# Kernel optimization log

Hardware: AMD Instinct MI355X
Metric: run time of the kernel (lower is better)

The kernel has to match this reference:

```python
import jax, jax.numpy as jnp
import numpy as np

N = 2048      # nodes (= in_features = out_features, forced by h0 @ adj)
C = 512       # channels
B = 8         # batch
NNZ = 65536   # number of edges (avg degree 32)
NEG = -9e15   # masked-fill value from the source


def setup_inputs() -> dict:
    key = jax.random.key(0)
    k1, k2, k3, k4 = jax.random.split(key, 4)
    x = jax.random.normal(k1, (B, C, N), dtype=jnp.float32)
    # xavier_normal_ with gain=0.01: std = gain * sqrt(2/(fan_in+fan_out))
    std = 0.01 * float(np.sqrt(2.0 / (N + N)))
    W1 = jax.random.normal(k2, (N, N), dtype=jnp.float32) * std
    W2 = jax.random.normal(k3, (N, N), dtype=jnp.float32) * std
    # e is initialized to 1 in the source; perturb so softmax is non-trivial
    e = 1.0 + 0.1 * jax.random.normal(k4, (NNZ,), dtype=jnp.float32)
    # flat row-major indices of mask nonzeros, unique + sorted (matches adj[mask] = e)
    rng = np.random.default_rng(0)
    edge_idx = np.sort(rng.choice(N * N, size=NNZ, replace=False)).astype(np.int64)
    return {"x": x, "W1": W1, "W2": W2, "e": e, "edge_idx": jnp.asarray(edge_idx)}


def reference(x, W1, W2, e, edge_idx):
    # h0, h1: [B, C, N]
    h0 = jnp.matmul(x, W1)
    h1 = jnp.matmul(x, W2)
    # scatter per-edge logits into dense [N, N], masked positions = -9e15
    logits = jnp.full((N * N,), NEG, dtype=jnp.float32).at[edge_idx].set(e)
    A = jax.nn.softmax(logits.reshape(N, N), axis=1)  # row-wise softmax
    diag = jnp.diagonal(A)                 # A * I  (self term, diagonal scaling)
    A_off = A - jnp.diag(diag)             # A * (1 - I)  (neighbor term)
    # h0 @ (A*I) == h0 scaled per-node by diag; h1 @ (A*(1-I)) dense GEMM
    out = h0 * diag[None, None, :] + jnp.matmul(h1, A_off)
    return out  # [B, C, N]; torch squeeze is a no-op here; bias=False
```

## Files before the change

kernel.cpp:

```cpp
#include <hip/hip_runtime.h>
#include <hip/hip_bf16.h>
#include <stdint.h>

#define NN 2048
#define LOG2NN 11
#define GK 2048
#define GNC 2048

typedef __bf16 bf16x8 __attribute__((ext_vector_type(8)));
typedef float f32x4 __attribute__((ext_vector_type(4)));

__device__ __forceinline__ ushort f2bf(float f) {
  uint32_t x = __float_as_uint(f);
  uint32_t r = (x + 0x7fffu + ((x >> 16) & 1u)) >> 16;
  return (ushort)r;
}

__global__ __launch_bounds__(256) void prep_kernel(
    const float* __restrict__ W1, const float* __restrict__ W2,
    ushort* __restrict__ WT, ushort* __restrict__ W2T,
    const float* __restrict__ x, ushort* __restrict__ xb,
    int* __restrict__ hist, float* __restrict__ uW, int* __restrict__ ecnt) {
  __shared__ float tile[64][65];
  const int bid = blockIdx.x;
  const int t = threadIdx.x;
  if (bid < 2048) {
    const int m = bid >> 10;
    const int rem = bid & 1023;
    const int r0 = (rem >> 5) * 64, c0 = (rem & 31) * 64;
    const float* in = m ? W2 : W1;
    ushort* out = m ? W2T : WT;
    const int tx = t & 15, ty = t >> 4;
#pragma unroll
    for (int i = 0; i < 4; ++i) {
      int r = i * 16 + ty;
      float4 v = *reinterpret_cast<const float4*>(&in[(size_t)(r0 + r) * NN + c0 + tx * 4]);
      tile[r][tx * 4 + 0] = v.x;
      tile[r][tx * 4 + 1] = v.y;
      tile[r][tx * 4 + 2] = v.z;
      tile[r][tx * 4 + 3] = v.w;
    }
    __syncthreads();
#pragma unroll
    for (int i = 0; i < 4; ++i) {
      int oc = i * 16 + ty;
      ushort4 o;
      o.x = f2bf(tile[tx * 4 + 0][oc]);
      o.y = f2bf(tile[tx * 4 + 1][oc]);
      o.z = f2bf(tile[tx * 4 + 2][oc]);
      o.w = f2bf(tile[tx * 4 + 3][oc]);
      *reinterpret_cast<ushort4*>(&out[(size_t)(c0 + oc) * NN + r0 + tx * 4]) = o;
    }
  } else if (bid < 6144) {
    int i = (bid - 2048) * 256 + t;
    const float4* in4 = reinterpret_cast<const float4*>(x);
    float4 a = in4[2 * i];
    float4 b = in4[2 * i + 1];
    uint4 o;
    o.x = (uint32_t)f2bf(a.x) | ((uint32_t)f2bf(a.y) << 16);
    o.y = (uint32_t)f2bf(a.z) | ((uint32_t)f2bf(a.w) << 16);
    o.z = (uint32_t)f2bf(b.x) | ((uint32_t)f2bf(b.y) << 16);
    o.w = (uint32_t)f2bf(b.z) | ((uint32_t)f2bf(b.w) << 16);
    reinterpret_cast<uint4*>(xb)[i] = o;
  } else {
#pragma unroll
    for (int j = 0; j < 8; ++j) {
      hist[t * 8 + j] = 0;
      uW[t * 8 + j] = 0.f;
    }
    if (t == 0) *ecnt = 0;
  }
}

__device__ __forceinline__ int lower_bound32(const int* __restrict__ a, int n, int v) {
  int lo = 0, hi = n;
  while (lo < hi) {
    int mid = (lo + hi) >> 1;
    if (a[mid] < v) lo = mid + 1; else hi = mid;
  }
  return lo;
}

__global__ __launch_bounds__(256) void softmax_hist_kernel(
    const int* __restrict__ idx, const float* __restrict__ e, int nnz,
    float* __restrict__ vals, float* __restrict__ diag, int* __restrict__ empty,
    int* __restrict__ ecnt, int* __restrict__ hist) {
  const int w = threadIdx.x >> 6, lane = threadIdx.x & 63;
  const int r = blockIdx.x * 4 + w;
  int lo = lower_bound32(idx, nnz, r << LOG2NN);
  int hi = lower_bound32(idx, nnz, (r + 1) << LOG2NN);
  if (hi <= lo) {
    if (lane == 0) { diag[r] = 1.0f / NN; empty[r] = 1; atomicAdd(ecnt, 1); }
    return;
  }
  float m = -3.0e38f;
  for (int j = lo + lane; j < hi; j += 64) m = fmaxf(m, e[j]);
#pragma unroll
  for (int s = 32; s >= 1; s >>= 1) m = fmaxf(m, __shfl_xor(m, s));
  float sum = 0.f;
  for (int j = lo + lane; j < hi; j += 64) sum += expf(e[j] - m);
#pragma unroll
  for (int s = 32; s >= 1; s >>= 1) sum += __shfl_xor(sum, s);
  float inv = 1.0f / sum;
  float dv = 0.f;
  for (int j = lo + lane; j < hi; j += 64) {
    float v = expf(e[j] - m) * inv;
    vals[j] = v;
    int c = idx[j] & (NN - 1);
    if (c == r) dv = v;
    else atomicAdd(&hist[c], 1);
  }
#pragma unroll
  for (int s = 32; s >= 1; s >>= 1) dv += __shfl_xor(dv, s);
  if (lane == 0) { diag[r] = dv; empty[r] = 0; }
}

__global__ __launch_bounds__(256) void scan_uw_kernel(
    const int* __restrict__ hist, int* __restrict__ base, int* __restrict__ cursor,
    const float* __restrict__ W2, const int* __restrict__ empty,
    const int* __restrict__ ecnt, float* __restrict__ uW) {
  if (blockIdx.x == 0) {
    const int l = threadIdx.x;
    if (l >= 64) return;
    int vals[32], pre[32];
    int run = 0;
#pragma unroll
    for (int j = 0; j < 32; ++j) {
      vals[j] = hist[l * 32 + j];
      pre[j] = run;
      run += vals[j];
    }
    int tot = run, inc = run;
#pragma unroll
    for (int s = 1; s < 64; s <<= 1) {
      int o = __shfl_up(inc, s);
      if (l >= s) inc += o;
    }
    int excl = inc - tot;
#pragma unroll
    for (int j = 0; j < 32; ++j) {
      int b = excl + pre[j];
      base[l * 32 + j] = b;
      cursor[l * 32 + j] = b;
    }
  } else {
    if (*ecnt == 0) return;
    int p = (blockIdx.x - 1) * 256 + threadIdx.x;
    float s = 0.f;
    for (int k = 0; k < NN; ++k)
      if (empty[k]) s += W2[(size_t)p * NN + k];
    uW[p] = s * (1.0f / NN);
  }
}

__global__ void scatter_kernel(const int* __restrict__ idx, const float* __restrict__ vals,
                               int nnz, int* __restrict__ cursor,
                               int* __restrict__ ek, float* __restrict__ ev) {
  int j = blockIdx.x * blockDim.x + threadIdx.x;
  if (j >= nnz) return;
  int f = idx[j];
  int c = f & (NN - 1), r = f >> LOG2NN;
  if (c != r) {
    int p = atomicAdd(&cursor[c], 1);
    ek[p] = r;
    ev[p] = vals[j];
  }
}

__global__ __launch_bounds__(256) void spmm_kernel(
    const int* __restrict__ ek, const float* __restrict__ ev,
    const int* __restrict__ base, const int* __restrict__ hist,
    const ushort* __restrict__ W2T,
    const float* __restrict__ diag, const int* __restrict__ empty,
    const float* __restrict__ uW, ushort* WT) {
  const int w = threadIdx.x >> 6, lane = threadIdx.x & 63;
  const int n = blockIdx.x * 2 + (w >> 1);
  const int c0 = (w & 1) * 1024 + lane * 16;
  const int start = base[n], cnt = hist[n];
  float acc[2][8];
#pragma unroll
  for (int g = 0; g < 2; ++g) {
    float4 u0 = *reinterpret_cast<const float4*>(&uW[c0 + g * 8]);
    float4 u1 = *reinterpret_cast<const float4*>(&uW[c0 + g * 8 + 4]);
    acc[g][0] = u0.x; acc[g][1] = u0.y; acc[g][2] = u0.z; acc[g][3] = u0.w;
    acc[g][4] = u1.x; acc[g][5] = u1.y; acc[g][6] = u1.z; acc[g][7] = u1.w;
  }
  float d = diag[n];
  if (d != 0.f) {
#pragma unroll
    for (int g = 0; g < 2; ++g) {
      bf16x8 wd = *reinterpret_cast<const bf16x8*>(&WT[(size_t)n * NN + c0 + g * 8]);
#pragma unroll
      for (int j = 0; j < 8; ++j) acc[g][j] += d * (float)wd[j];
    }
  }
  int i = 0;
  for (; i + 4 <= cnt; i += 4) {
    int k[4];
    float v[4];
    bf16x8 wv[4][2];
#pragma unroll
    for (int e2 = 0; e2 < 4; ++e2) {
      k[e2] = ek[start + i + e2];
      v[e2] = ev[start + i + e2];
    }
#pragma unroll
    for (int e2 = 0; e2 < 4; ++e2)
#pragma unroll
      for (int g = 0; g < 2; ++g)
        wv[e2][g] = *reinterpret_cast<const bf16x8*>(&W2T[(size_t)k[e2] * NN + c0 + g * 8]);
#pragma unroll
    for (int e2 = 0; e2 < 4; ++e2)
#pragma unroll
      for (int g = 0; g < 2; ++g)
#pragma unroll
        for (int j = 0; j < 8; ++j)
          acc[g][j] += v[e2] * (float)wv[e2][g][j];
  }
  for (; i < cnt; ++i) {
    int k0 = ek[start + i];
    float v0 = ev[start + i];
#pragma unroll
    for (int g = 0; g < 2; ++g) {
      bf16x8 w0 = *reinterpret_cast<const bf16x8*>(&W2T[(size_t)k0 * NN + c0 + g * 8]);
#pragma unroll
      for (int j = 0; j < 8; ++j) acc[g][j] += v0 * (float)w0[j];
    }
  }
  if (empty[n]) {
#pragma unroll
    for (int g = 0; g < 2; ++g) {
      bf16x8 we = *reinterpret_cast<const bf16x8*>(&W2T[(size_t)n * NN + c0 + g * 8]);
#pragma unroll
      for (int j = 0; j < 8; ++j) acc[g][j] -= (1.0f / NN) * (float)we[j];
    }
  }
#pragma unroll
  for (int g = 0; g < 2; ++g) {
    uint4 o;
    o.x = (uint32_t)f2bf(acc[g][0]) | ((uint32_t)f2bf(acc[g][1]) << 16);
    o.y = (uint32_t)f2bf(acc[g][2]) | ((uint32_t)f2bf(acc[g][3]) << 16);
    o.z = (uint32_t)f2bf(acc[g][4]) | ((uint32_t)f2bf(acc[g][5]) << 16);
    o.w = (uint32_t)f2bf(acc[g][6]) | ((uint32_t)f2bf(acc[g][7]) << 16);
    *reinterpret_cast<uint4*>(&WT[(size_t)n * NN + c0 + g * 8]) = o;
  }
}

__device__ __forceinline__ void gload_lds16(const ushort* g, char* l) {
  __builtin_amdgcn_global_load_lds(
      (__attribute__((address_space(1))) uint32_t*)(uintptr_t)g,
      (__attribute__((address_space(3))) uint32_t*)l, 16, 0, 0);
}

#define NT 32

__global__ __launch_bounds__(512, 2)
void gemm8_kernel(const ushort* __restrict__ A, const ushort* __restrict__ Bt,
                  float* __restrict__ Cf) {
  __shared__ __align__(16) char smem[98304];
  const int t = threadIdx.x;
  const int wid = t >> 6, lane = t & 63;
  const int wm = wid >> 2, wn = wid & 3;
  const int fr = lane & 15, fg = lane >> 4;

  const int swz = ((int)blockIdx.x & 7) * 32 + ((int)blockIdx.x >> 3);
  const int m0 = (swz >> 4) * 256;
  const int n0 = (swz & 15) * 128;

  const int l8 = lane >> 3;
  const int scol = ((lane & 7) ^ l8) << 3;
  const int srow = wid * 8 + l8;

#define STGA(H, TAU) do {                                                      \
    const int _b = (TAU) & 1;                                                  \
    gload_lds16(A + (size_t)(m0 + (H) * 128 + srow) * GK + (TAU) * 64 + scol,  \
                smem + _b * 32768 + (H) * 16384 + wid * 1024);                 \
    gload_lds16(A + (size_t)(m0 + (H) * 128 + 64 + srow) * GK + (TAU) * 64 + scol, \
                smem + _b * 32768 + (H) * 16384 + 8192 + wid * 1024);          \
  } while (0)

#define STGB(TAU) do {                                                         \
    const int _b = (TAU) & 1;                                                  \
    gload_lds16(Bt + (size_t)(n0 + srow) * GK + (TAU) * 64 + scol,             \
                smem + 65536 + _b * 16384 + wid * 1024);                       \
    gload_lds16(Bt + (size_t)(n0 + 64 + srow) * GK + (TAU) * 64 + scol,        \
                smem + 65536 + _b * 16384 + 8192 + wid * 1024);                \
  } while (0)

  const int sw = (fr & 7) << 4;
  const int ko0 = (fg * 16) ^ sw;
  const int ko1 = (64 + fg * 16) ^ sw;
  const int arow = (wm * 16 + fr) * 128;
  const int brow = (wn * 32 + fr) * 128;

  f32x4 acc[2][4][2] = {};
  bf16x8 aF[4][2], bF[2][2];

#define LDA(MQ, B_) do {                                                       \
    _Pragma("unroll") for (int mf = 0; mf < 4; ++mf) {                         \
      const char* _p = smem + (B_) * 32768 + arow + ((MQ) * 128 + mf * 32) * 128; \
      aF[mf][0] = *reinterpret_cast<const bf16x8*>(_p + ko0);                  \
      aF[mf][1] = *reinterpret_cast<const bf16x8*>(_p + ko1);                  \
    }                                                                          \
  } while (0)

#define LDB(B_) do {                                                           \
    _Pragma("unroll") for (int nf = 0; nf < 2; ++nf) {                         \
      const char* _p = smem + 65536 + (B_) * 16384 + brow + (nf * 16) * 128;   \
      bF[nf][0] = *reinterpret_cast<const bf16x8*>(_p + ko0);                  \
      bF[nf][1] = *reinterpret_cast<const bf16x8*>(_p + ko1);                  \
    }                                                                          \
  } while (0)

#define MM(MQ) do {                                                            \
    _Pragma("unroll") for (int mf = 0; mf < 4; ++mf)                           \
      _Pragma("unroll") for (int nf = 0; nf < 2; ++nf) {                       \
        acc[MQ][mf][nf] = __builtin_amdgcn_mfma_f32_16x16x32_bf16(             \
            aF[mf][0], bF[nf][0], acc[MQ][mf][nf], 0, 0, 0);                   \
        acc[MQ][mf][nf] = __builtin_amdgcn_mfma_f32_16x16x32_bf16(             \
            aF[mf][1], bF[nf][1], acc[MQ][mf][nf], 0, 0, 0);                   \
      }                                                                        \
  } while (0)

#define PHASE_MID() do {                                                       \
    __builtin_amdgcn_s_barrier();                                              \
    asm volatile("s_waitcnt lgkmcnt(0)" ::: "memory");                         \
    __builtin_amdgcn_sched_barrier(0);                                         \
    __builtin_amdgcn_s_setprio(1);                                             \
  } while (0)

#define PHASE_END() do {                                                       \
    __builtin_amdgcn_s_setprio(0);                                             \
    __builtin_amdgcn_s_barrier();                                              \
  } while (0)

  STGA(0, 0); STGA(1, 0); STGB(0);
  STGB(1); STGA(0, 1);
  asm volatile("s_waitcnt vmcnt(4)" ::: "memory");
  __builtin_amdgcn_sched_barrier(0);
  __builtin_amdgcn_s_barrier();

  for (int kt = 0; kt < NT; ++kt) {
    const int b = kt & 1;
    const int t1 = (kt + 1) & (NT - 1), t2 = (kt + 2) & (NT - 1);
    LDA(0, b); LDB(b);
    STGA(1, t1);
    PHASE_MID(); MM(0); PHASE_END();
    LDA(1, b);
    STGB(t2); STGA(0, t2);
    PHASE_MID(); MM(1);
    __builtin_amdgcn_s_setprio(0);
    asm volatile("s_waitcnt vmcnt(4)" ::: "memory");
    __builtin_amdgcn_sched_barrier(0);
    __builtin_amdgcn_s_barrier();
  }

  asm volatile("s_waitcnt vmcnt(0)" ::: "memory");
  const int cr = lane >> 4, cc = lane & 15;
#pragma unroll
  for (int mq = 0; mq < 2; ++mq)
#pragma unroll
    for (int mf = 0; mf < 4; ++mf)
#pragma unroll
      for (int nf = 0; nf < 2; ++nf)
#pragma unroll
        for (int q = 0; q < 4; ++q) {
          int gm = m0 + mq * 128 + mf * 32 + wm * 16 + cr * 4 + q;
          int gn = n0 + wn * 32 + nf * 16 + cc;
          Cf[(size_t)gm * GNC + gn] = acc[mq][mf][nf][q];
        }
}

extern "C" void kernel_launch(void* const* d_in, const int* in_sizes, int n_in,
                              void* d_out, int out_size, void* d_ws, size_t ws_size,
                              hipStream_t stream) {
  const float* x   = (const float*)d_in[0];
  const float* W1  = (const float*)d_in[1];
  const float* W2  = (const float*)d_in[2];
  const float* e   = (const float*)d_in[3];
  const int*   eix = (const int*)d_in[4];
  const int nnz = in_sizes[3];
  float* out = (float*)d_out;

  char* w = (char*)d_ws;
  ushort* W2T  = (ushort*)w; w += (size_t)NN * NN * 2;
  ushort* WT   = (ushort*)w; w += (size_t)NN * NN * 2;
  ushort* xb   = (ushort*)w; w += (size_t)4096 * NN * 2;
  float*  vals = (float*)w;  w += (size_t)nnz * 4;
  int*    ek   = (int*)w;    w += (size_t)nnz * 4;
  float*  ev   = (float*)w;  w += (size_t)nnz * 4;
  int*    hist = (int*)w;    w += NN * 4;
  int*    base = (int*)w;    w += NN * 4;
  int*    curs = (int*)w;    w += NN * 4;
  float*  diag = (float*)w;  w += NN * 4;
  int*    empt = (int*)w;    w += NN * 4;
  float*  uW   = (float*)w;  w += NN * 4;
  int*    ecnt = (int*)w;    w += 256;

  prep_kernel<<<dim3(6145), dim3(256), 0, stream>>>(W1, W2, WT, W2T, x, xb,
                                                    hist, uW, ecnt);
  softmax_hist_kernel<<<dim3(512), dim3(256), 0, stream>>>(eix, e, nnz, vals,
                                                           diag, empt, ecnt, hist);
  scan_uw_kernel<<<dim3(9), dim3(256), 0, stream>>>(hist, base, curs, W2, empt,
                                                    ecnt, uW);
  scatter_kernel<<<dim3((nnz + 255) / 256), dim3(256), 0, stream>>>(eix, vals, nnz,
                                                                    curs, ek, ev);
  spmm_kernel<<<dim3(1024), dim3(256), 0, stream>>>(ek, ev, base, hist, W2T,
                                                    diag, empt, uW, WT);
  gemm8_kernel<<<dim3(256), dim3(512), 0, stream>>>(xb, WT, out);
}
```

Measured before the change: 109.7 us.

## Fuse softmax into prep kernel, move x conversion into spmm, restructure GEMM warp tiling

The row-softmax/histogram work moves into the prep kernel as extra blocks, and the zeroing of hist, uW and ecnt becomes a single memset. The x-to-bf16 conversion moves out of prep and into extra blocks of the spmm kernel, dropping one launch and letting that conversion run alongside the sparse work. The GEMM main loop changes from a two-phase split with finer barriers to one loop per k-tile, with each wave computing a 64x64 sub-tile (4x4 MFMA fragments) instead of 2x(4x2). It loads then waits for the next stage only after the compute, which gives up some of the earlier overlap between loads and MFMAs.

```diff
diff --git a/kernel.cpp b/kernel.cpp
--- a/kernel.cpp
+++ b/kernel.cpp
@@ -16,11 +16,21 @@
   return (ushort)r;
 }
 
+__device__ __forceinline__ int lower_bound32(const int* __restrict__ a, int n, int v) {
+  int lo = 0, hi = n;
+  while (lo < hi) {
+    int mid = (lo + hi) >> 1;
+    if (a[mid] < v) lo = mid + 1; else hi = mid;
+  }
+  return lo;
+}
+
 __global__ __launch_bounds__(256) void prep_kernel(
     const float* __restrict__ W1, const float* __restrict__ W2,
     ushort* __restrict__ WT, ushort* __restrict__ W2T,
-    const float* __restrict__ x, ushort* __restrict__ xb,
-    int* __restrict__ hist, float* __restrict__ uW, int* __restrict__ ecnt) {
+    int* __restrict__ hist, int* __restrict__ ecnt,
+    const int* __restrict__ idx, const float* __restrict__ e, int nnz,
+    float* __restrict__ vals, float* __restrict__ diag, int* __restrict__ empty) {
   __shared__ float tile[64][65];
   const int bid = blockIdx.x;
   const int t = threadIdx.x;
@@ -51,68 +61,36 @@
       o.w = f2bf(tile[tx * 4 + 3][oc]);
       *reinterpret_cast<ushort4*>(&out[(size_t)(c0 + oc) * NN + r0 + tx * 4]) = o;
     }
-  } else if (bid < 6144) {
-    int i = (bid - 2048) * 256 + t;
-    const float4* in4 = reinterpret_cast<const float4*>(x);
-    float4 a = in4[2 * i];
-    float4 b = in4[2 * i + 1];
-    uint4 o;
-    o.x = (uint32_t)f2bf(a.x) | ((uint32_t)f2bf(a.y) << 16);
-    o.y = (uint32_t)f2bf(a.z) | ((uint32_t)f2bf(a.w) << 16);
-    o.z = (uint32_t)f2bf(b.x) | ((uint32_t)f2bf(b.y) << 16);
-    o.w = (uint32_t)f2bf(b.z) | ((uint32_t)f2bf(b.w) << 16);
-    reinterpret_cast<uint4*>(xb)[i] = o;
   } else {
-#pragma unroll
-    for (int j = 0; j < 8; ++j) {
-      hist[t * 8 + j] = 0;
-      uW[t * 8 + j] = 0.f;
-    }
-    if (t == 0) *ecnt = 0;
-  }
-}
-
-__device__ __forceinline__ int lower_bound32(const int* __restrict__ a, int n, int v) {
-  int lo = 0, hi = n;
-  while (lo < hi) {
-    int mid = (lo + hi) >> 1;
-    if (a[mid] < v) lo = mid + 1; else hi = mid;
-  }
-  return lo;
-}
-
-__global__ __launch_bounds__(256) void softmax_hist_kernel(
-    const int* __restrict__ idx, const float* __restrict__ e, int nnz,
-    float* __restrict__ vals, float* __restrict__ diag, int* __restrict__ empty,
-    int* __restrict__ ecnt, int* __restrict__ hist) {
-  const int w = threadIdx.x >> 6, lane = threadIdx.x & 63;
-  const int r = blockIdx.x * 4 + w;
-  int lo = lower_bound32(idx, nnz, r << LOG2NN);
-  int hi = lower_bound32(idx, nnz, (r + 1) << LOG2NN);
-  if (hi <= lo) {
-    if (lane == 0) { diag[r] = 1.0f / NN; empty[r] = 1; atomicAdd(ecnt, 1); }
-    return;
-  }
-  float m = -3.0e38f;
-  for (int j = lo + lane; j < hi; j += 64) m = fmaxf(m, e[j]);
-#pragma unroll
-  for (int s = 32; s >= 1; s >>= 1) m = fmaxf(m, __shfl_xor(m, s));
-  float sum = 0.f;
-  for (int j = lo + lane; j < hi; j += 64) sum += expf(e[j] - m);
-#pragma unroll
-  for (int s = 32; s >= 1; s >>= 1) sum += __shfl_xor(sum, s);
-  float inv = 1.0f / sum;
-  float dv = 0.f;
-  for (int j = lo + lane; j < hi; j += 64) {
-    float v = expf(e[j] - m) * inv;
-    vals[j] = v;
-    int c = idx[j] & (NN - 1);
-    if (c == r) dv = v;
-    else atomicAdd(&hist[c], 1);
-  }
-#pragma unroll
-  for (int s = 32; s >= 1; s >>= 1) dv += __shfl_xor(dv, s);
-  if (lane == 0) { diag[r] = dv; empty[r] = 0; }
+    const int w = t >> 6, lane = t & 63;
+    const int r = (bid - 2048) * 4 + w;
+    int lo = lower_bound32(idx, nnz, r << LOG2NN);
+    int hi = lower_bound32(idx, nnz, (r + 1) << LOG2NN);
+    if (hi <= lo) {
+      if (lane == 0) { diag[r] = 1.0f / NN; empty[r] = 1; atomicAdd(ecnt, 1); }
+      return;
+    }
+    float m = -3.0e38f;
+    for (int j = lo + lane; j < hi; j += 64) m = fmaxf(m, e[j]);
+#pragma unroll
+    for (int s = 32; s >= 1; s >>= 1) m = fmaxf(m, __shfl_xor(m, s));
+    float sum = 0.f;
+    for (int j = lo + lane; j < hi; j += 64) sum += expf(e[j] - m);
+#pragma unroll
+    for (int s = 32; s >= 1; s >>= 1) sum += __shfl_xor(sum, s);
+    float inv = 1.0f / sum;
+    float dv = 0.f;
+    for (int j = lo + lane; j < hi; j += 64) {
+      float v = expf(e[j] - m) * inv;
+      vals[j] = v;
+      int c = idx[j] & (NN - 1);
+      if (c == r) dv = v;
+      else atomicAdd(&hist[c], 1);
+    }
+#pragma unroll
+    for (int s = 32; s >= 1; s >>= 1) dv += __shfl_xor(dv, s);
+    if (lane == 0) { diag[r] = dv; empty[r] = 0; }
+  }
 }
 
 __global__ __launch_bounds__(256) void scan_uw_kernel(
@@ -172,7 +150,21 @@
     const int* __restrict__ base, const int* __restrict__ hist,
     const ushort* __restrict__ W2T,
     const float* __restrict__ diag, const int* __restrict__ empty,
-    const float* __restrict__ uW, ushort* WT) {
+    const float* __restrict__ uW, ushort* WT,
+    const float* __restrict__ x, ushort* __restrict__ xb) {
+  if (blockIdx.x >= 1024) {
+    int i = ((int)blockIdx.x - 1024) * 256 + threadIdx.x;
+    const float4* in4 = reinterpret_cast<const float4*>(x);
+    float4 a = in4[2 * i];
+    float4 b = in4[2 * i + 1];
+    uint4 o;
+    o.x = (uint32_t)f2bf(a.x) | ((uint32_t)f2bf(a.y) << 16);
+    o.y = (uint32_t)f2bf(a.z) | ((uint32_t)f2bf(a.w) << 16);
+    o.z = (uint32_t)f2bf(b.x) | ((uint32_t)f2bf(b.y) << 16);
+    o.w = (uint32_t)f2bf(b.z) | ((uint32_t)f2bf(b.w) << 16);
+    reinterpret_cast<uint4*>(xb)[i] = o;
+    return;
+  }
   const int w = threadIdx.x >> 6, lane = threadIdx.x & 63;
   const int n = blockIdx.x * 2 + (w >> 1);
   const int c0 = (w & 1) * 1024 + lane * 16;
@@ -260,7 +252,7 @@
   __shared__ __align__(16) char smem[98304];
   const int t = threadIdx.x;
   const int wid = t >> 6, lane = t & 63;
-  const int wm = wid >> 2, wn = wid & 3;
+  const int wm = wid >> 1, wn = wid & 1;
   const int fr = lane & 15, fg = lane >> 4;
 
   const int swz = ((int)blockIdx.x & 7) * 32 + ((int)blockIdx.x >> 3);
@@ -290,85 +282,77 @@
   const int sw = (fr & 7) << 4;
   const int ko0 = (fg * 16) ^ sw;
   const int ko1 = (64 + fg * 16) ^ sw;
-  const int arow = (wm * 16 + fr) * 128;
-  const int brow = (wn * 32 + fr) * 128;
-
-  f32x4 acc[2][4][2] = {};
-  bf16x8 aF[4][2], bF[2][2];
-
-#define LDA(MQ, B_) do {                                                       \
-    _Pragma("unroll") for (int mf = 0; mf < 4; ++mf) {                         \
-      const char* _p = smem + (B_) * 32768 + arow + ((MQ) * 128 + mf * 32) * 128; \
-      aF[mf][0] = *reinterpret_cast<const bf16x8*>(_p + ko0);                  \
-      aF[mf][1] = *reinterpret_cast<const bf16x8*>(_p + ko1);                  \
-    }                                                                          \
-  } while (0)
-
-#define LDB(B_) do {                                                           \
-    _Pragma("unroll") for (int nf = 0; nf < 2; ++nf) {                         \
-      const char* _p = smem + 65536 + (B_) * 16384 + brow + (nf * 16) * 128;   \
-      bF[nf][0] = *reinterpret_cast<const bf16x8*>(_p + ko0);                  \
-      bF[nf][1] = *reinterpret_cast<const bf16x8*>(_p + ko1);                  \
-    }                                                                          \
-  } while (0)
-
-#define MM(MQ) do {                                                            \
-    _Pragma("unroll") for (int mf = 0; mf < 4; ++mf)                           \
-      _Pragma("unroll") for (int nf = 0; nf < 2; ++nf) {                       \
-        acc[MQ][mf][nf] = __builtin_amdgcn_mfma_f32_16x16x32_bf16(             \
-            aF[mf][0], bF[nf][0], acc[MQ][mf][nf], 0, 0, 0);                   \
-        acc[MQ][mf][nf] = __builtin_amdgcn_mfma_f32_16x16x32_bf16(             \
-            aF[mf][1], bF[nf][1], acc[MQ][mf][nf], 0, 0, 0);                   \
-      }                                                                        \
-  } while (0)
-
-#define PHASE_MID() do {                                                       \
-    __builtin_amdgcn_s_barrier();                                              \
-    asm volatile("s_waitcnt lgkmcnt(0)" ::: "memory");                         \
-    __builtin_amdgcn_sched_barrier(0);                                         \
-    __builtin_amdgcn_s_setprio(1);                                             \
-  } while (0)
-
-#define PHASE_END() do {                                                       \
-    __builtin_amdgcn_s_setprio(0);                                             \
-    __builtin_amdgcn_s_barrier();                                              \
-  } while (0)
+
+  f32x4 acc[4][4] = {};
 
   STGA(0, 0); STGA(1, 0); STGB(0);
-  STGB(1); STGA(0, 1);
-  asm volatile("s_waitcnt vmcnt(4)" ::: "memory");
-  __builtin_amdgcn_sched_barrier(0);
+  STGA(0, 1); STGA(1, 1); STGB(1);
+  asm volatile("s_waitcnt vmcnt(6)" ::: "memory");
   __builtin_amdgcn_s_barrier();
+  asm volatile("" ::: "memory");
 
   for (int kt = 0; kt < NT; ++kt) {
     const int b = kt & 1;
-    const int t1 = (kt + 1) & (NT - 1), t2 = (kt + 2) & (NT - 1);
-    LDA(0, b); LDB(b);
-    STGA(1, t1);
-    PHASE_MID(); MM(0); PHASE_END();
-    LDA(1, b);
-    STGB(t2); STGA(0, t2);
-    PHASE_MID(); MM(1);
+    const int t2 = (kt + 2) & (NT - 1);
+    const char* Ab = smem + b * 32768;
+    const char* Bb = smem + 65536 + b * 16384;
+    bf16x8 aF[4][2], bF[4][2];
+#pragma unroll
+    for (int mf = 0; mf < 4; ++mf) {
+      const int row = wm * 64 + mf * 16 + fr;
+      const char* p = Ab + (row >> 7) * 16384 + (row & 127) * 128;
+      aF[mf][0] = *reinterpret_cast<const bf16x8*>(p + ko0);
+    }
+#pragma unroll
+    for (int nf = 0; nf < 4; ++nf) {
+      const char* p = Bb + (wn * 64 + nf * 16 + fr) * 128;
+      bF[nf][0] = *reinterpret_cast<const bf16x8*>(p + ko0);
+    }
+#pragma unroll
+    for (int mf = 0; mf < 4; ++mf) {
+      const int row = wm * 64 + mf * 16 + fr;
+      const char* p = Ab + (row >> 7) * 16384 + (row & 127) * 128;
+      aF[mf][1] = *reinterpret_cast<const bf16x8*>(p + ko1);
+    }
+#pragma unroll
+    for (int nf = 0; nf < 4; ++nf) {
+      const char* p = Bb + (wn * 64 + nf * 16 + fr) * 128;
+      bF[nf][1] = *reinterpret_cast<const bf16x8*>(p + ko1);
+    }
+    __builtin_amdgcn_s_setprio(1);
+#pragma unroll
+    for (int mf = 0; mf < 4; ++mf)
+#pragma unroll
+      for (int nf = 0; nf < 4; ++nf)
+        acc[mf][nf] = __builtin_amdgcn_mfma_f32_16x16x32_bf16(
+            aF[mf][0], bF[nf][0], acc[mf][nf], 0, 0, 0);
+#pragma unroll
+    for (int mf = 0; mf < 4; ++mf)
+#pragma unroll
+      for (int nf = 0; nf < 4; ++nf)
+        acc[mf][nf] = __builtin_amdgcn_mfma_f32_16x16x32_bf16(
+            aF[mf][1], bF[nf][1], acc[mf][nf], 0, 0, 0);
     __builtin_amdgcn_s_setprio(0);
-    asm volatile("s_waitcnt vmcnt(4)" ::: "memory");
-    __builtin_amdgcn_sched_barrier(0);
     __builtin_amdgcn_s_barrier();
+    asm volatile("" ::: "memory");
+    STGA(0, t2); STGA(1, t2); STGB(t2);
+    asm volatile("s_waitcnt vmcnt(6)" ::: "memory");
+    __builtin_amdgcn_s_barrier();
+    asm volatile("" ::: "memory");
   }
 
   asm volatile("s_waitcnt vmcnt(0)" ::: "memory");
   const int cr = lane >> 4, cc = lane & 15;
 #pragma unroll
-  for (int mq = 0; mq < 2; ++mq)
-#pragma unroll
-    for (int mf = 0; mf < 4; ++mf)
-#pragma unroll
-      for (int nf = 0; nf < 2; ++nf)
-#pragma unroll
-        for (int q = 0; q < 4; ++q) {
-          int gm = m0 + mq * 128 + mf * 32 + wm * 16 + cr * 4 + q;
-          int gn = n0 + wn * 32 + nf * 16 + cc;
-          Cf[(size_t)gm * GNC + gn] = acc[mq][mf][nf][q];
-        }
+  for (int mf = 0; mf < 4; ++mf)
+#pragma unroll
+    for (int nf = 0; nf < 4; ++nf)
+#pragma unroll
+      for (int q = 0; q < 4; ++q) {
+        int gm = m0 + wm * 64 + mf * 16 + cr * 4 + q;
+        int gn = n0 + wn * 64 + nf * 16 + cc;
+        Cf[(size_t)gm * GNC + gn] = acc[mf][nf][q];
+      }
 }
 
 extern "C" void kernel_launch(void* const* d_in, const int* in_sizes, int n_in,
@@ -389,23 +373,24 @@
   float*  vals = (float*)w;  w += (size_t)nnz * 4;
   int*    ek   = (int*)w;    w += (size_t)nnz * 4;
   float*  ev   = (float*)w;  w += (size_t)nnz * 4;
-  int*    hist = (int*)w;    w += NN * 4;
   int*    base = (int*)w;    w += NN * 4;
   int*    curs = (int*)w;    w += NN * 4;
   float*  diag = (float*)w;  w += NN * 4;
   int*    empt = (int*)w;    w += NN * 4;
+  int*    hist = (int*)w;    w += NN * 4;
   float*  uW   = (float*)w;  w += NN * 4;
   int*    ecnt = (int*)w;    w += 256;
 
-  prep_kernel<<<dim3(6145), dim3(256), 0, stream>>>(W1, W2, WT, W2T, x, xb,
-                                                    hist, uW, ecnt);
-  softmax_hist_kernel<<<dim3(512), dim3(256), 0, stream>>>(eix, e, nnz, vals,
-                                                           diag, empt, ecnt, hist);
+  hipMemsetAsync(hist, 0, NN * 4 + NN * 4 + 256, stream);
+
+  prep_kernel<<<dim3(2560), dim3(256), 0, stream>>>(W1, W2, WT, W2T,
+                                                    hist, ecnt,
+                                                    eix, e, nnz, vals, diag, empt);
   scan_uw_kernel<<<dim3(9), dim3(256), 0, stream>>>(hist, base, curs, W2, empt,
                                                     ecnt, uW);
   scatter_kernel<<<dim3((nnz + 255) / 256), dim3(256), 0, stream>>>(eix, vals, nnz,
                                                                     curs, ek, ev);
-  spmm_kernel<<<dim3(1024), dim3(256), 0, stream>>>(ek, ev, base, hist, W2T,
-                                                    diag, empt, uW, WT);
+  spmm_kernel<<<dim3(5120), dim3(256), 0, stream>>>(ek, ev, base, hist, W2T,
+                                                    diag, empt, uW, WT, x, xb);
   gemm8_kernel<<<dim3(256), dim3(512), 0, stream>>>(xb, WT, out);
 }
```

Result: no change. 111.2 us (+1.4%).
